# Performance work log

Measured on AMD Instinct MI355X. Metric: run time of the kernel, lower is better.

The kernel has to match this reference:

```python
import jax, jax.numpy as jnp
import numpy as np
from jax.scipy.special import gammaln

N = 8388608      # batch size
TMAX = 256       # exclusive upper bound on poisson event counts (targets in [0, TMAX))


def setup_inputs() -> dict:
    key = jax.random.key(0)
    k1, k2, k3 = jax.random.split(key, 3)
    # lambda (poisson rate) must be strictly positive for log(lam); uniform in [0.5, 5.0]
    inputs = jax.random.uniform(k1, (N, 1), jnp.float32, 0.5, 5.0)
    targets = jax.random.randint(k2, (N,), 0, TMAX, jnp.int32)
    risk = jax.random.randint(k3, (N,), 0, 2, jnp.int32)
    return {"inputs": inputs, "targets": targets, "risk": risk}


def reference(inputs, targets, risk):
    # Poisson branch of LogLikelihoodLossWithCensoring.
    # Original: surv[i] = sum_{j=0}^{t_i} [1 - (-lam_i + j*log(lam_i) - lgamma(j+1))]
    #                  = (t_i+1)*(1+lam_i) - log(lam_i)*t_i*(t_i+1)/2 + sum_{j=0}^{t_i} lgamma(j+1)
    # The per-sample double Python loop is replaced by a cumsum table + gather.
    lam = inputs[:, 0]                                   # [N]
    t = targets.astype(jnp.float32)                      # [N]
    log_lam = jnp.log(lam)

    j = jnp.arange(TMAX + 1, dtype=jnp.float32)          # [TMAX+1]
    lgam_cumsum = jnp.cumsum(gammaln(j + 1.0))           # c[k] = sum_{j=0}^{k} lgamma(j+1)

    surv = (t + 1.0) * (1.0 + lam) - log_lam * t * (t + 1.0) * 0.5 + lgam_cumsum[targets]
    loglikelihood = t * log_lam - lam - gammaln(t + 1.0)

    loss_ll = -jnp.sum(jnp.where(risk == 1, loglikelihood, surv))
    return loss_ll / inputs.shape[0]
```

## Files before the change

### kernel.cpp

```cpp
#include <hip/hip_runtime.h>
#include <math.h>

#define NELEM  8388608
#define GRID   2048
#define BLOCK  256
#define NVEC   (NELEM / 4)
#define STRIDE (GRID * BLOCK)

__global__ __launch_bounds__(BLOCK) void loss_fused(
    const float4* __restrict__ lam4,
    const int4*   __restrict__ tgt4,
    const int4*   __restrict__ risk4,
    unsigned int* __restrict__ flags,
    unsigned long long* __restrict__ partials,
    float*        __restrict__ out)
{
    __shared__ float2 tab[512];
    __shared__ float  woff[4];
    __shared__ double wsum[4];

    const int tid  = threadIdx.x;
    const int lane = tid & 63;
    const int wid  = tid >> 6;

    {
        float tf = (float)tid;
        float v  = lgammaf(tf + 1.0f);
        float scan = v;
        #pragma unroll
        for (int d = 1; d < 64; d <<= 1) {
            float n = __shfl_up(scan, d, 64);
            if (lane >= d) scan += n;
        }
        if (lane == 63) woff[wid] = scan;
        __syncthreads();
        float off = 0.f;
        for (int w = 0; w < wid; ++w) off += woff[w];
        float csum = scan + off;
        tab[(tid << 1) | 1] = make_float2(tf, -v);
        tab[(tid << 1)]     = make_float2(-tf * (tf + 1.0f) * 0.5f,
                                          (tf + 1.0f) + csum);
    }
    __syncthreads();

    const int base = blockIdx.x * BLOCK + tid;
    double acc = 0.0;

    #define ONE(la_, t_, r_, g_) {                                   \
        float  la = (la_);                                           \
        int    t  = (t_);                                            \
        float  tf = (float)t;                                        \
        float  a  = ((r_) == 1) ? -1.0f : (tf + 1.0f);               \
        float2 c  = tab[(t << 1) | (r_)];                            \
        float  ll = __logf(la);                                      \
        g_ += fmaf(a, la, fmaf(c.x, ll, c.y));                       \
    }
    #define GROUP(L, T, R) {                                         \
        float g = 0.f;                                               \
        ONE(L.x, T.x, R.x, g);                                       \
        ONE(L.y, T.y, R.y, g);                                       \
        ONE(L.z, T.z, R.z, g);                                       \
        ONE(L.w, T.w, R.w, g);                                       \
        acc += (double)g;                                            \
    }

    float4 L0 = lam4[base];              int4 T0 = tgt4[base];              int4 R0 = risk4[base];
    float4 L1 = lam4[base + STRIDE];     int4 T1 = tgt4[base + STRIDE];     int4 R1 = risk4[base + STRIDE];
    GROUP(L0, T0, R0);
    float4 L2 = lam4[base + 2 * STRIDE]; int4 T2 = tgt4[base + 2 * STRIDE]; int4 R2 = risk4[base + 2 * STRIDE];
    GROUP(L1, T1, R1);
    float4 L3 = lam4[base + 3 * STRIDE]; int4 T3 = tgt4[base + 3 * STRIDE]; int4 R3 = risk4[base + 3 * STRIDE];
    GROUP(L2, T2, R2);
    GROUP(L3, T3, R3);
    #undef GROUP
    #undef ONE

    #pragma unroll
    for (int d = 32; d > 0; d >>= 1) acc += __shfl_down(acc, d, 64);
    if (lane == 0) wsum[wid] = acc;
    __syncthreads();

    if (tid == 0) {
        double total = wsum[0] + wsum[1] + wsum[2] + wsum[3];
        __hip_atomic_store(&partials[blockIdx.x], (unsigned long long)__double_as_longlong(total),
                           __ATOMIC_RELAXED, __HIP_MEMORY_SCOPE_AGENT);
        asm volatile("s_waitcnt vmcnt(0)" ::: "memory");
        __hip_atomic_store(&flags[blockIdx.x], 1u,
                           __ATOMIC_RELAXED, __HIP_MEMORY_SCOPE_AGENT);
    }

    if (blockIdx.x == 0) {
        __syncthreads();
        double s = 0.0;
        #pragma unroll
        for (int i = tid; i < GRID; i += BLOCK) {
            while (__hip_atomic_load(&flags[i], __ATOMIC_RELAXED,
                                     __HIP_MEMORY_SCOPE_AGENT) == 0u)
                __builtin_amdgcn_s_sleep(1);
            unsigned long long b = __hip_atomic_load(&partials[i], __ATOMIC_RELAXED,
                                                     __HIP_MEMORY_SCOPE_AGENT);
            s += __longlong_as_double((long long)b);
        }
        #pragma unroll
        for (int d = 32; d > 0; d >>= 1) s += __shfl_down(s, d, 64);
        if (lane == 0) wsum[wid] = s;
        __syncthreads();
        if (tid == 0) {
            double tot = wsum[0] + wsum[1] + wsum[2] + wsum[3];
            out[0] = (float)(-tot / (double)NELEM);
        }
    }
}

extern "C" void kernel_launch(void* const* d_in, const int* in_sizes, int n_in,
                              void* d_out, int out_size, void* d_ws, size_t ws_size,
                              hipStream_t stream)
{
    const float4* lam4  = (const float4*)d_in[0];
    const int4*   tgt4  = (const int4*)d_in[1];
    const int4*   risk4 = (const int4*)d_in[2];
    unsigned int*       flags    = (unsigned int*)d_ws;
    unsigned long long* partials = (unsigned long long*)((char*)d_ws + 8192);
    float*              out      = (float*)d_out;

    hipMemsetAsync(d_ws, 0, 8192, stream);
    loss_fused<<<GRID, BLOCK, 0, stream>>>(lam4, tgt4, risk4, flags, partials, out);
}
```

Baseline: 28.02 us.

## Split fused spin-wait reduction into main kernel plus separate finalize kernel

Replaces the single-kernel design, where block 0 spin-waited on per-block flags, with two launches. The main kernel writes per-block double partials and a one-block finalize kernel sums them. This drops the hipMemsetAsync and the spin-wait, which could stall block 0 and hold its CU. In exchange it adds a second kernel launch and the gap between the two kernels.

```diff
diff --git a/kernel.cpp b/kernel.cpp
--- a/kernel.cpp
+++ b/kernel.cpp
@@ -7,13 +7,11 @@
 #define NVEC   (NELEM / 4)
 #define STRIDE (GRID * BLOCK)
 
-__global__ __launch_bounds__(BLOCK) void loss_fused(
+__global__ __launch_bounds__(BLOCK) void loss_main(
     const float4* __restrict__ lam4,
     const int4*   __restrict__ tgt4,
     const int4*   __restrict__ risk4,
-    unsigned int* __restrict__ flags,
-    unsigned long long* __restrict__ partials,
-    float*        __restrict__ out)
+    double*       __restrict__ partials)
 {
     __shared__ float2 tab[512];
     __shared__ float  woff[4];
@@ -79,36 +77,29 @@
     for (int d = 32; d > 0; d >>= 1) acc += __shfl_down(acc, d, 64);
     if (lane == 0) wsum[wid] = acc;
     __syncthreads();
+    if (tid == 0)
+        partials[blockIdx.x] = wsum[0] + wsum[1] + wsum[2] + wsum[3];
+}
 
+__global__ __launch_bounds__(256) void loss_finalize(
+    const double* __restrict__ partials, float* __restrict__ out)
+{
+    const int tid  = threadIdx.x;
+    const int lane = tid & 63;
+    const int wid  = tid >> 6;
+    __shared__ double ws[4];
+
+    double acc = 0.0;
+    #pragma unroll
+    for (int i = 0; i < GRID / 256; ++i)
+        acc += partials[tid + i * 256];
+    #pragma unroll
+    for (int d = 32; d > 0; d >>= 1) acc += __shfl_down(acc, d, 64);
+    if (lane == 0) ws[wid] = acc;
+    __syncthreads();
     if (tid == 0) {
-        double total = wsum[0] + wsum[1] + wsum[2] + wsum[3];
-        __hip_atomic_store(&partials[blockIdx.x], (unsigned long long)__double_as_longlong(total),
-                           __ATOMIC_RELAXED, __HIP_MEMORY_SCOPE_AGENT);
-        asm volatile("s_waitcnt vmcnt(0)" ::: "memory");
-        __hip_atomic_store(&flags[blockIdx.x], 1u,
-                           __ATOMIC_RELAXED, __HIP_MEMORY_SCOPE_AGENT);
-    }
-
-    if (blockIdx.x == 0) {
-        __syncthreads();
-        double s = 0.0;
-        #pragma unroll
-        for (int i = tid; i < GRID; i += BLOCK) {
-            while (__hip_atomic_load(&flags[i], __ATOMIC_RELAXED,
-                                     __HIP_MEMORY_SCOPE_AGENT) == 0u)
-                __builtin_amdgcn_s_sleep(1);
-            unsigned long long b = __hip_atomic_load(&partials[i], __ATOMIC_RELAXED,
-                                                     __HIP_MEMORY_SCOPE_AGENT);
-            s += __longlong_as_double((long long)b);
-        }
-        #pragma unroll
-        for (int d = 32; d > 0; d >>= 1) s += __shfl_down(s, d, 64);
-        if (lane == 0) wsum[wid] = s;
-        __syncthreads();
-        if (tid == 0) {
-            double tot = wsum[0] + wsum[1] + wsum[2] + wsum[3];
-            out[0] = (float)(-tot / (double)NELEM);
-        }
+        double s = ws[0] + ws[1] + ws[2] + ws[3];
+        out[0] = (float)(-s / (double)NELEM);
     }
 }
 
@@ -119,10 +110,9 @@
     const float4* lam4  = (const float4*)d_in[0];
     const int4*   tgt4  = (const int4*)d_in[1];
     const int4*   risk4 = (const int4*)d_in[2];
-    unsigned int*       flags    = (unsigned int*)d_ws;
-    unsigned long long* partials = (unsigned long long*)((char*)d_ws + 8192);
-    float*              out      = (float*)d_out;
+    double* partials    = (double*)d_ws;
+    float*  out         = (float*)d_out;
 
-    hipMemsetAsync(d_ws, 0, 8192, stream);
-    loss_fused<<<GRID, BLOCK, 0, stream>>>(lam4, tgt4, risk4, flags, partials, out);
+    loss_main<<<GRID, BLOCK, 0, stream>>>(lam4, tgt4, risk4, partials);
+    loss_finalize<<<1, 256, 0, stream>>>(partials, out);
 }
```

Measured after the change: 24.50 us. 1.14x faster.
